# Kernel optimization log

Hardware: AMD Instinct MI355X
Metric: run time of the kernel (lower is better)

## Reference

```python
import jax, jax.numpy as jnp
import numpy as np

BATCH, N, NX, NU, NY = 64, 4096, 128, 32, 32


def setup_inputs() -> dict:
    key = jax.random.key(0)
    k1, k2, k3, k4, k5 = jax.random.split(key, 5)
    # A scaled to spectral radius ~0.9 so the recurrence is stable (module has is_stable()).
    A = jax.random.normal(k1, (NX, NX), jnp.float32) * (0.9 / np.sqrt(NX).astype(np.float32))
    B = jax.random.normal(k2, (NX, NU), jnp.float32) * (1.0 / np.sqrt(NU).astype(np.float32))
    C = jax.random.normal(k3, (NY, NX), jnp.float32) * (1.0 / np.sqrt(NX).astype(np.float32))
    D = jax.random.normal(k4, (NY, NU), jnp.float32) * (1.0 / np.sqrt(NU).astype(np.float32))
    d = jax.random.normal(k5, (BATCH, N, NU, 1), jnp.float32)
    return {"d": d, "A": A, "B": B, "C": C, "D": D}


def reference(d, A, B, C, D):
    # d: [batch, N, nu, 1]. LTI recurrence: x_{k+1} = A x_k + B u_k ; y_k = C x_k + D u_k, x_0 = 0.
    u = jnp.swapaxes(d[..., 0], 0, 1)  # [N, batch, nu] time-major for scan
    x0 = jnp.zeros((d.shape[0], A.shape[0]), d.dtype)  # [batch, nx]

    def step(x, uk):
        y = x @ C.T + uk @ D.T          # [batch, ny] uses pre-update state x_k
        x_next = x @ A.T + uk @ B.T     # [batch, nx]
        return x_next, (y, x)

    xN, (ys, xs) = jax.lax.scan(step, x0, u)
    y = jnp.swapaxes(ys, 0, 1)[..., None]                      # [batch, N, ny, 1]
    x = jnp.swapaxes(xs, 0, 1)                                 # [batch, N, nx] = x_0..x_{N-1}
    x = jnp.concatenate([x, xN[:, None]], axis=1)[..., None]   # [batch, N+1, nx, 1]
    return y, (x,)
```

## Files before the change

### kernel.cpp

```cpp
#include <hip/hip_runtime.h>
#include <stdint.h>
#include <stddef.h>

typedef short s8v   __attribute__((ext_vector_type(8)));
typedef float f32x4 __attribute__((ext_vector_type(4)));

union BF8 { s8v v; unsigned short u[8]; };

__device__ __forceinline__ float bf16_f(unsigned short h) {
  unsigned u = ((unsigned)h) << 16;
  return __builtin_bit_cast(float, u);
}
__device__ __forceinline__ void split_trunc(float x, unsigned short &h, unsigned short &l) {
  unsigned u = __builtin_bit_cast(unsigned, x);
  h = (unsigned short)(u >> 16);
  float hi = __builtin_bit_cast(float, u & 0xFFFF0000u);
  float r = x - hi;
  l = (unsigned short)(__builtin_bit_cast(unsigned, r) >> 16);
}
__device__ __forceinline__ f32x4 mfma16(s8v a, s8v b, f32x4 c) {
  return __builtin_amdgcn_mfma_f32_16x16x32_bf16(a, b, c, 0, 0, 0);
}
__device__ __forceinline__ void split8(f32x4 a, f32x4 b, s8v &h, s8v &l) {
  BF8 hh, ll;
  #pragma unroll
  for (int i = 0; i < 4; ++i) { split_trunc(a[i], hh.u[i], ll.u[i]); split_trunc(b[i], hh.u[4 + i], ll.u[4 + i]); }
  h = hh.v; l = ll.v;
}

#define BATCH 64
#define NN    4096
#define NX    128
#define NU    32
#define NY    32
#define LPAD  132
#define CH    32
#define CPB   128

#define OFF_AH   0
#define OFF_AL   32768
#define OFF_BH   65536
#define OFF_BL   73728
#define OFF_CH   81920
#define OFF_CL   90112
#define OFF_DH   98304
#define OFF_DL   100352
#define OFF_A2H  102400
#define OFF_A2L  135168
#define OFF_ABH  167936
#define OFF_ABL  176128
#define OFF_G1H  184320
#define OFF_G1L  217088
#define OFF_G2H  249856
#define OFF_G2L  282624
#define OFF_G3H  315392
#define OFF_G3L  348160
#define OFF_P0   380928
#define OFF_P1   446464
#define OFF_V    512000
#define OFF_S    4706304

__global__ void k_mm_conv(const float* __restrict__ A, const float* __restrict__ B,
                          const float* __restrict__ C, const float* __restrict__ D,
                          float* __restrict__ P, unsigned short* A2h, unsigned short* A2l,
                          unsigned short* Ah, unsigned short* Al,
                          unsigned short* Bh, unsigned short* Bl,
                          unsigned short* Ch, unsigned short* Cl,
                          unsigned short* Dh, unsigned short* Dl) {
  int gid = blockIdx.x * 256 + threadIdx.x;
  if (blockIdx.x < 64) {
    int row = gid >> 7, col = gid & 127;
    const float* xr = A + row * 128;
    float a0 = 0.f, a1 = 0.f;
    #pragma unroll 8
    for (int k = 0; k < 128; k += 2) {
      a0 = fmaf(xr[k],     A[k * 128 + col],       a0);
      a1 = fmaf(xr[k + 1], A[(k + 1) * 128 + col], a1);
    }
    float acc = a0 + a1;
    P[gid] = acc;
    unsigned short h, l; split_trunc(acc, h, l);
    A2h[gid] = h; A2l[gid] = l;
  } else {
    int idx = gid - 16384;
    unsigned short h, l;
    if (idx < 16384)      { split_trunc(A[idx], h, l); Ah[idx] = h; Al[idx] = l; }
    else if (idx < 20480) { int i = idx - 16384; split_trunc(B[i], h, l); Bh[i] = h; Bl[i] = l; }
    else if (idx < 24576) { int i = idx - 20480; split_trunc(C[i], h, l); Ch[i] = h; Cl[i] = l; }
    else if (idx < 25600) { int i = idx - 24576; split_trunc(D[i], h, l); Dh[i] = h; Dl[i] = l; }
  }
}

__global__ void k_mm128(const float* __restrict__ X, const float* __restrict__ Y,
                        float* __restrict__ Z, unsigned short* Zh, unsigned short* Zl,
                        int writeBF) {
  int gid = blockIdx.x * 256 + threadIdx.x;
  int row = gid >> 7, col = gid & 127;
  const float* xr = X + row * 128;
  float a0 = 0.f, a1 = 0.f;
  #pragma unroll 8
  for (int k = 0; k < 128; k += 2) {
    a0 = fmaf(xr[k],     Y[k * 128 + col],       a0);
    a1 = fmaf(xr[k + 1], Y[(k + 1) * 128 + col], a1);
  }
  float acc = a0 + a1;
  Z[gid] = acc;
  if (writeBF) { unsigned short h, l; split_trunc(acc, h, l); Zh[gid] = h; Zl[gid] = l; }
}

__global__ void k_ab(const float* __restrict__ A, const float* __restrict__ B,
                     unsigned short* ABh, unsigned short* ABl) {
  int gid = blockIdx.x * 256 + threadIdx.x;
  int row = gid >> 5, col = gid & 31;
  float acc = 0.f;
  #pragma unroll 8
  for (int k = 0; k < 128; ++k) acc = fmaf(A[row * 128 + k], B[k * 32 + col], acc);
  unsigned short h, l; split_trunc(acc, h, l);
  ABh[gid] = h; ABl[gid] = l;
}

__global__ __launch_bounds__(256, 2) void k_pass1(
    const float* __restrict__ d,
    const unsigned short* __restrict__ A2h, const unsigned short* __restrict__ A2l,
    const unsigned short* __restrict__ ABh, const unsigned short* __restrict__ ABl,
    const unsigned short* __restrict__ Bh,  const unsigned short* __restrict__ Bl,
    float* __restrict__ vout) {
  __shared__ unsigned short Xh[2][16][LPAD];
  __shared__ unsigned short Xl[2][16][LPAD];
  const int tid = threadIdx.x;
  const int w = tid >> 6, l = tid & 63, q = l >> 4, m = l & 15;
  const int g = blockIdx.x;

  s8v fA2h[2][4], fA2l[2][4], fABh[2], fABl[2], fBh[2], fBl[2];
  #pragma unroll
  for (int t2 = 0; t2 < 2; ++t2) {
    const int n = (2 * w + t2) * 16 + m;
    #pragma unroll
    for (int kt = 0; kt < 4; ++kt) {
      const int k0 = kt * 32 + q * 8;
      fA2h[t2][kt] = *(const s8v*)(A2h + n * 128 + k0);
      fA2l[t2][kt] = *(const s8v*)(A2l + n * 128 + k0);
    }
    fABh[t2] = *(const s8v*)(ABh + n * 32 + q * 8);
    fABl[t2] = *(const s8v*)(ABl + n * 32 + q * 8);
    fBh[t2]  = *(const s8v*)(Bh  + n * 32 + q * 8);
    fBl[t2]  = *(const s8v*)(Bl  + n * 32 + q * 8);
  }
  for (int i = tid; i < 16 * LPAD; i += 256) {
    ((unsigned short*)Xh[0])[i] = 0;
    ((unsigned short*)Xl[0])[i] = 0;
  }
  __syncthreads();

  const int ch = g * 16 + m, b = ch >> 7, chunk = ch & (CPB - 1);
  const float* ubase = d + ((size_t)b * NN + chunk * CH) * NU + q * 8;

  f32x4 cu[4];
  cu[0] = *(const f32x4*)(ubase);      cu[1] = *(const f32x4*)(ubase + 4);
  cu[2] = *(const f32x4*)(ubase + 32); cu[3] = *(const f32x4*)(ubase + 36);

  f32x4 acc[2];
  #pragma unroll 2
  for (int r = 0; r < 16; ++r) {
    const int p = r & 1;
    f32x4 nu0 = cu[0], nu1 = cu[1], nu2 = cu[2], nu3 = cu[3];
    if (r < 15) {
      const float* up = ubase + (size_t)(2 * r + 2) * NU;
      nu0 = *(const f32x4*)up;        nu1 = *(const f32x4*)(up + 4);
      nu2 = *(const f32x4*)(up + 32); nu3 = *(const f32x4*)(up + 36);
    }
    s8v u0h, u0l, u1h, u1l;
    split8(cu[0], cu[1], u0h, u0l);
    split8(cu[2], cu[3], u1h, u1l);
    s8v fXh[4], fXl[4];
    #pragma unroll
    for (int kt = 0; kt < 4; ++kt) {
      fXh[kt] = *(const s8v*)&Xh[p][m][kt * 32 + q * 8];
      fXl[kt] = *(const s8v*)&Xl[p][m][kt * 32 + q * 8];
    }
    #pragma unroll
    for (int t2 = 0; t2 < 2; ++t2) {
      f32x4 a0 = {0.f,0.f,0.f,0.f}, a1 = {0.f,0.f,0.f,0.f}, a2 = {0.f,0.f,0.f,0.f};
      #pragma unroll
      for (int kt = 0; kt < 4; ++kt) a0 = mfma16(fXh[kt], fA2h[t2][kt], a0);
      a0 = mfma16(u0h, fABh[t2], a0);
      a0 = mfma16(u1h, fBh[t2],  a0);
      #pragma unroll
      for (int kt = 0; kt < 4; ++kt) a1 = mfma16(fXl[kt], fA2h[t2][kt], a1);
      a1 = mfma16(u0l, fABh[t2], a1);
      a1 = mfma16(u1l, fBh[t2],  a1);
      #pragma unroll
      for (int kt = 0; kt < 4; ++kt) a2 = mfma16(fXh[kt], fA2l[t2][kt], a2);
      a2 = mfma16(u0h, fABl[t2], a2);
      a2 = mfma16(u1h, fBl[t2],  a2);
      acc[t2] = a0 + a1 + a2;
    }
    if (r < 15) {
      #pragma unroll
      for (int t2 = 0; t2 < 2; ++t2) {
        const int col = (2 * w + t2) * 16 + m;
        #pragma unroll
        for (int rr = 0; rr < 4; ++rr) {
          unsigned short h, lo;
          split_trunc(acc[t2][rr], h, lo);
          Xh[1 - p][q * 4 + rr][col] = h;
          Xl[1 - p][q * 4 + rr][col] = lo;
        }
      }
      __syncthreads();
      cu[0] = nu0; cu[1] = nu1; cu[2] = nu2; cu[3] = nu3;
    }
  }
  #pragma unroll
  for (int t2 = 0; t2 < 2; ++t2) {
    const int col = (2 * w + t2) * 16 + m;
    #pragma unroll
    for (int rr = 0; rr < 4; ++rr) {
      const int row = g * 16 + q * 4 + rr;
      vout[(size_t)row * 128 + col] = acc[t2][rr];
    }
  }
}

__global__ __launch_bounds__(256, 1) void k_carry(
    const unsigned short* __restrict__ G1h, const unsigned short* __restrict__ G1l,
    const unsigned short* __restrict__ G2h, const unsigned short* __restrict__ G2l,
    const unsigned short* __restrict__ G3h, const unsigned short* __restrict__ G3l,
    const float* __restrict__ v, float* __restrict__ sout) {
  const int tid = threadIdx.x;
  const int w = tid >> 6, l = tid & 63, q = l >> 4, m = l & 15;
  const int g = blockIdx.x;
  const int chm = g * 16 + m, cm = chm & (CPB - 1);

  f32x4 a[2];
  a[0] = (f32x4){0.f,0.f,0.f,0.f};
  a[1] = (f32x4){0.f,0.f,0.f,0.f};

#define CARRY_TERM(GH, GL, DELTA)                                              \
  {                                                                            \
    const s8v zero = {0,0,0,0,0,0,0,0};                                        \
    s8v vh[4], vl[4];                                                          \
    _Pragma("unroll")                                                          \
    for (int kt = 0; kt < 4; ++kt) {                                           \
      if (cm >= DELTA) {                                                       \
        const float* vp = v + (size_t)(chm - DELTA) * NX + kt * 32 + q * 8;    \
        split8(*(const f32x4*)vp, *(const f32x4*)(vp + 4), vh[kt], vl[kt]);    \
      } else { vh[kt] = zero; vl[kt] = zero; }                                 \
    }                                                                          \
    _Pragma("unroll")                                                          \
    for (int t2 = 0; t2 < 2; ++t2) {                                           \
      const int n = (2 * w + t2) * 16 + m;                                     \
      _Pragma("unroll")                                                        \
      for (int kt = 0; kt < 4; ++kt) {                                         \
        const int k0 = kt * 32 + q * 8;                                        \
        s8v gh = *(const s8v*)(GH + n * NX + k0);                              \
        s8v gl = *(const s8v*)(GL + n * NX + k0);                              \
        a[t2] = mfma16(vh[kt], gh, a[t2]);                                     \
        a[t2] = mfma16(vl[kt], gh, a[t2]);                                     \
        a[t2] = mfma16(vh[kt], gl, a[t2]);                                     \
      }                                                                        \
    }                                                                          \
  }

  CARRY_TERM(G1h, G1l, 2)
  CARRY_TERM(G2h, G2l, 3)
  CARRY_TERM(G3h, G3l, 4)
#undef CARRY_TERM

  #pragma unroll
  for (int t2 = 0; t2 < 2; ++t2) {
    const int col = (2 * w + t2) * 16 + m;
    #pragma unroll
    for (int rr = 0; rr < 4; ++rr) {
      const int chr = g * 16 + q * 4 + rr, cr = chr & (CPB - 1);
      float sv = 0.f;
      if (cr >= 1) sv = a[t2][rr] + v[(size_t)(chr - 1) * NX + col];
      sout[(size_t)chr * NX + col] = sv;
    }
  }
}

__global__ __launch_bounds__(256, 2) void k_scan2(
    const float* __restrict__ d, const float* __restrict__ s,
    const unsigned short* __restrict__ Ah, const unsigned short* __restrict__ Al,
    const unsigned short* __restrict__ Bh, const unsigned short* __restrict__ Bl,
    const unsigned short* __restrict__ Ch, const unsigned short* __restrict__ Cl,
    const unsigned short* __restrict__ Dh, const unsigned short* __restrict__ Dl,
    float* __restrict__ yout, float* __restrict__ xout) {
  __shared__ unsigned short Eh[16][LPAD];
  __shared__ unsigned short El[16][LPAD];
  __shared__ unsigned short Oh[16][LPAD];
  __shared__ unsigned short Ol[16][LPAD];
  const int tid = threadIdx.x;
  const int w = tid >> 6, l = tid & 63, q = l >> 4, m = l & 15;
  const int g = blockIdx.x;

  s8v fAh[2][4], fAl[2][4], fBh[2], fBl[2];
  #pragma unroll
  for (int t2 = 0; t2 < 2; ++t2) {
    const int n = (2 * w + t2) * 16 + m;
    #pragma unroll
    for (int kt = 0; kt < 4; ++kt) {
      const int k0 = kt * 32 + q * 8;
      fAh[t2][kt] = *(const s8v*)(Ah + n * 128 + k0);
      fAl[t2][kt] = *(const s8v*)(Al + n * 128 + k0);
    }
    fBh[t2] = *(const s8v*)(Bh + n * 32 + q * 8);
    fBl[t2] = *(const s8v*)(Bl + n * 32 + q * 8);
  }
  s8v fCh[4], fCl[4], fDh, fDl;
  {
    const int o = (w & 1) * 16 + m;
    #pragma unroll
    for (int kt = 0; kt < 4; ++kt) {
      const int k0 = kt * 32 + q * 8;
      fCh[kt] = *(const s8v*)(Ch + o * 128 + k0);
      fCl[kt] = *(const s8v*)(Cl + o * 128 + k0);
    }
    fDh = *(const s8v*)(Dh + o * 32 + q * 8);
    fDl = *(const s8v*)(Dl + o * 32 + q * 8);
  }

  {
    const int lb = tid >> 4, i0 = (tid & 15) * 8;
    const int chS = g * 16 + lb, bS = chS >> 7, cS = chS & (CPB - 1);
    const float* sp = s + (size_t)chS * 128 + i0;
    f32x4 s0 = *(const f32x4*)sp, s1 = *(const f32x4*)(sp + 4);
    s8v hh, ll;
    split8(s0, s1, hh, ll);
    *(s8v*)&Eh[lb][i0] = hh;
    *(s8v*)&El[lb][i0] = ll;
    float* xp = xout + ((size_t)bS * (NN + 1) + (size_t)cS * CH) * NX + i0;
    *(f32x4*)xp = s0;
    *(f32x4*)(xp + 4) = s1;
  }
  __syncthreads();

  const int ch = g * 16 + m, b = ch >> 7, chunk = ch & (CPB - 1);
  const float* ubase = d + ((size_t)b * NN + chunk * CH) * NU + q * 8;

  float* xptr[2][4];
  bool xlast[2][4];
  float* yptr[4];
  #pragma unroll
  for (int t2 = 0; t2 < 2; ++t2) {
    const int col = (2 * w + t2) * 16 + m;
    #pragma unroll
    for (int rr = 0; rr < 4; ++rr) {
      const int chX = g * 16 + q * 4 + rr, bX = chX >> 7, cX = chX & (CPB - 1);
      xptr[t2][rr] = xout + ((size_t)bX * (NN + 1) + (size_t)cX * CH + 1) * NX + col;
      xlast[t2][rr] = (cX == CPB - 1);
    }
  }
  #pragma unroll
  for (int rr = 0; rr < 4; ++rr) {
    const int chY = g * 16 + q * 4 + rr, bY = chY >> 7, cY = chY & (CPB - 1);
    yptr[rr] = yout + ((size_t)bY * NN + (size_t)cY * CH) * NY + (w & 1) * 16 + m;
  }

  f32x4 cu[4];
  cu[0] = *(const f32x4*)(ubase);      cu[1] = *(const f32x4*)(ubase + 4);
  cu[2] = *(const f32x4*)(ubase + 32); cu[3] = *(const f32x4*)(ubase + 36);

  #pragma unroll 1
  for (int r = 0; r < 16; ++r) {
    f32x4 nu0 = cu[0], nu1 = cu[1], nu2 = cu[2], nu3 = cu[3];
    if (r < 15) {
      const float* up = ubase + (size_t)(2 * r + 2) * NU;
      nu0 = *(const f32x4*)up;        nu1 = *(const f32x4*)(up + 4);
      nu2 = *(const f32x4*)(up + 32); nu3 = *(const f32x4*)(up + 36);
    }
    s8v u0h, u0l;
    split8(cu[0], cu[1], u0h, u0l);
    s8v fXh[4], fXl[4];
    #pragma unroll
    for (int kt = 0; kt < 4; ++kt) {
      fXh[kt] = *(const s8v*)&Eh[m][kt * 32 + q * 8];
      fXl[kt] = *(const s8v*)&El[m][kt * 32 + q * 8];
    }
    f32x4 xo[2];
    #pragma unroll
    for (int t2 = 0; t2 < 2; ++t2) {
      f32x4 a0 = {0.f,0.f,0.f,0.f}, a1 = {0.f,0.f,0.f,0.f}, a2 = {0.f,0.f,0.f,0.f};
      #pragma unroll
      for (int kt = 0; kt < 4; ++kt) a0 = mfma16(fXh[kt], fAh[t2][kt], a0);
      a0 = mfma16(u0h, fBh[t2], a0);
      #pragma unroll
      for (int kt = 0; kt < 4; ++kt) a1 = mfma16(fXl[kt], fAh[t2][kt], a1);
      a1 = mfma16(u0l, fBh[t2], a1);
      #pragma unroll
      for (int kt = 0; kt < 4; ++kt) a2 = mfma16(fXh[kt], fAl[t2][kt], a2);
      a2 = mfma16(u0h, fBl[t2], a2);
      xo[t2] = a0 + a1 + a2;
    }
    if (w < 2) {
      f32x4 b0 = {0.f,0.f,0.f,0.f}, b1 = {0.f,0.f,0.f,0.f}, b2 = {0.f,0.f,0.f,0.f};
      #pragma unroll
      for (int kt = 0; kt < 4; ++kt) b0 = mfma16(fXh[kt], fCh[kt], b0);
      b0 = mfma16(u0h, fDh, b0);
      #pragma unroll
      for (int kt = 0; kt < 4; ++kt) b1 = mfma16(fXl[kt], fCh[kt], b1);
      b1 = mfma16(u0l, fDh, b1);
      #pragma unroll
      for (int kt = 0; kt < 4; ++kt) b2 = mfma16(fXh[kt], fCl[kt], b2);
      b2 = mfma16(u0h, fDl, b2);
      f32x4 yv = b0 + b1 + b2;
      #pragma unroll
      for (int rr = 0; rr < 4; ++rr) *(yptr[rr]) = yv[rr];
    }
    #pragma unroll
    for (int t2 = 0; t2 < 2; ++t2) {
      const int col = (2 * w + t2) * 16 + m;
      #pragma unroll
      for (int rr = 0; rr < 4; ++rr) {
        *(xptr[t2][rr]) = xo[t2][rr];
        unsigned short h, lo;
        split_trunc(xo[t2][rr], h, lo);
        Oh[q * 4 + rr][col] = h;
        Ol[q * 4 + rr][col] = lo;
      }
    }
    __syncthreads();

    s8v u1h, u1l;
    split8(cu[2], cu[3], u1h, u1l);
    s8v fOh[4], fOl[4];
    #pragma unroll
    for (int kt = 0; kt < 4; ++kt) {
      fOh[kt] = *(const s8v*)&Oh[m][kt * 32 + q * 8];
      fOl[kt] = *(const s8v*)&Ol[m][kt * 32 + q * 8];
    }
    f32x4 xe[2];
    #pragma unroll
    for (int t2 = 0; t2 < 2; ++t2) {
      f32x4 a0 = {0.f,0.f,0.f,0.f}, a1 = {0.f,0.f,0.f,0.f}, a2 = {0.f,0.f,0.f,0.f};
      #pragma unroll
      for (int kt = 0; kt < 4; ++kt) a0 = mfma16(fOh[kt], fAh[t2][kt], a0);
      a0 = mfma16(u1h, fBh[t2], a0);
      #pragma unroll
      for (int kt = 0; kt < 4; ++kt) a1 = mfma16(fOl[kt], fAh[t2][kt], a1);
      a1 = mfma16(u1l, fBh[t2], a1);
      #pragma unroll
      for (int kt = 0; kt < 4; ++kt) a2 = mfma16(fOh[kt], fAl[t2][kt], a2);
      a2 = mfma16(u1h, fBl[t2], a2);
      xe[t2] = a0 + a1 + a2;
    }
    if (w >= 2) {
      f32x4 c0 = {0.f,0.f,0.f,0.f}, c1 = {0.f,0.f,0.f,0.f}, c2 = {0.f,0.f,0.f,0.f};
      #pragma unroll
      for (int kt = 0; kt < 4; ++kt) c0 = mfma16(fOh[kt], fCh[kt], c0);
      c0 = mfma16(u1h, fDh, c0);
      #pragma unroll
      for (int kt = 0; kt < 4; ++kt) c1 = mfma16(fOl[kt], fCh[kt], c1);
      c1 = mfma16(u1l, fDh, c1);
      #pragma unroll
      for (int kt = 0; kt < 4; ++kt) c2 = mfma16(fOh[kt], fCl[kt], c2);
      c2 = mfma16(u1h, fDl, c2);
      f32x4 yv = c0 + c1 + c2;
      #pragma unroll
      for (int rr = 0; rr < 4; ++rr) *(yptr[rr] + NY) = yv[rr];
    }
    #pragma unroll
    for (int t2 = 0; t2 < 2; ++t2) {
      const int col = (2 * w + t2) * 16 + m;
      #pragma unroll
      for (int rr = 0; rr < 4; ++rr) {
        if (r < 15 || xlast[t2][rr]) *(xptr[t2][rr] + NX) = xe[t2][rr];
        unsigned short h, lo;
        split_trunc(xe[t2][rr], h, lo);
        Eh[q * 4 + rr][col] = h;
        El[q * 4 + rr][col] = lo;
      }
    }
    __syncthreads();

    if (r < 15) {
      cu[0] = nu0; cu[1] = nu1; cu[2] = nu2; cu[3] = nu3;
      #pragma unroll
      for (int t2 = 0; t2 < 2; ++t2)
        #pragma unroll
        for (int rr = 0; rr < 4; ++rr) xptr[t2][rr] += 2 * NX;
      #pragma unroll
      for (int rr = 0; rr < 4; ++rr) yptr[rr] += 2 * NY;
    }
  }
}

extern "C" void kernel_launch(void* const* d_in, const int* in_sizes, int n_in,
                              void* d_out, int out_size, void* d_ws, size_t ws_size,
                              hipStream_t stream) {
  (void)in_sizes; (void)n_in; (void)out_size; (void)ws_size;
  const float* d = (const float*)d_in[0];
  const float* A = (const float*)d_in[1];
  const float* B = (const float*)d_in[2];
  const float* C = (const float*)d_in[3];
  const float* D = (const float*)d_in[4];

  char* ws = (char*)d_ws;
  unsigned short* Ah  = (unsigned short*)(ws + OFF_AH);
  unsigned short* Al  = (unsigned short*)(ws + OFF_AL);
  unsigned short* Bh  = (unsigned short*)(ws + OFF_BH);
  unsigned short* Bl  = (unsigned short*)(ws + OFF_BL);
  unsigned short* Chp = (unsigned short*)(ws + OFF_CH);
  unsigned short* Clp = (unsigned short*)(ws + OFF_CL);
  unsigned short* Dhp = (unsigned short*)(ws + OFF_DH);
  unsigned short* Dlp = (unsigned short*)(ws + OFF_DL);
  unsigned short* A2h = (unsigned short*)(ws + OFF_A2H);
  unsigned short* A2l = (unsigned short*)(ws + OFF_A2L);
  unsigned short* ABh = (unsigned short*)(ws + OFF_ABH);
  unsigned short* ABl = (unsigned short*)(ws + OFF_ABL);
  unsigned short* G1h = (unsigned short*)(ws + OFF_G1H);
  unsigned short* G1l = (unsigned short*)(ws + OFF_G1L);
  unsigned short* G2h = (unsigned short*)(ws + OFF_G2H);
  unsigned short* G2l = (unsigned short*)(ws + OFF_G2L);
  unsigned short* G3h = (unsigned short*)(ws + OFF_G3H);
  unsigned short* G3l = (unsigned short*)(ws + OFF_G3L);
  float* P0 = (float*)(ws + OFF_P0);
  float* P1 = (float*)(ws + OFF_P1);
  float* V  = (float*)(ws + OFF_V);
  float* S  = (float*)(ws + OFF_S);

  float* yout = (float*)d_out;
  float* xout = yout + (size_t)BATCH * NN * NY;

  k_mm_conv<<<164, 256, 0, stream>>>(A, B, C, D, P0, A2h, A2l,
                                     Ah, Al, Bh, Bl, Chp, Clp, Dhp, Dlp);
  k_ab<<<16, 256, 0, stream>>>(A, B, ABh, ABl);
  k_mm128<<<64, 256, 0, stream>>>(P0, P0, P1, nullptr, nullptr, 0);
  k_mm128<<<64, 256, 0, stream>>>(P1, P1, P0, nullptr, nullptr, 0);
  k_mm128<<<64, 256, 0, stream>>>(P0, P0, P1, nullptr, nullptr, 0);
  k_mm128<<<64, 256, 0, stream>>>(P1, P1, P0, G1h, G1l, 1);
  k_mm128<<<64, 256, 0, stream>>>(P0, P0, P1, G2h, G2l, 1);
  k_mm128<<<64, 256, 0, stream>>>(P0, P1, V,  G3h, G3l, 1);

  k_pass1<<<512, 256, 0, stream>>>(d, A2h, A2l, ABh, ABl, Bh, Bl, V);
  k_carry<<<512, 256, 0, stream>>>(G1h, G1l, G2h, G2l, G3h, G3l, V, S);
  k_scan2<<<512, 256, 0, stream>>>(d, S, Ah, Al, Bh, Bl, Chp, Clp, Dhp, Dlp,
                                   yout, xout);
}
```

Before: 290.3 us.

## Pre-split input into bf16 hi/lo buffers in a merged prep kernel

Adds a prep stage that converts the whole input d into bf16 hi/lo arrays once, and merges the old conversion and A*B kernels into that single launch. Both scan kernels now load pre-split u fragments, so the per-step split arithmetic inside the serial recurrence loops goes away. The cost is an extra full pass over d plus writing two bf16 copies, which keeps total traffic about the same but moves work off the latency-bound loops. k_carry's launch bounds are also raised to allow two blocks per CU.

```diff
diff --git a/kernel.cpp b/kernel.cpp
--- a/kernel.cpp
+++ b/kernel.cpp
@@ -59,16 +59,31 @@
 #define OFF_P1   446464
 #define OFF_V    512000
 #define OFF_S    4706304
-
-__global__ void k_mm_conv(const float* __restrict__ A, const float* __restrict__ B,
-                          const float* __restrict__ C, const float* __restrict__ D,
-                          float* __restrict__ P, unsigned short* A2h, unsigned short* A2l,
-                          unsigned short* Ah, unsigned short* Al,
-                          unsigned short* Bh, unsigned short* Bl,
-                          unsigned short* Ch, unsigned short* Cl,
-                          unsigned short* Dh, unsigned short* Dl) {
-  int gid = blockIdx.x * 256 + threadIdx.x;
-  if (blockIdx.x < 64) {
+#define OFF_UH   8900608
+#define OFF_UL   25677824
+
+__global__ void k_prep(const float* __restrict__ A, const float* __restrict__ B,
+                       const float* __restrict__ C, const float* __restrict__ D,
+                       const float* __restrict__ d,
+                       float* __restrict__ P, unsigned short* A2h, unsigned short* A2l,
+                       unsigned short* Ah, unsigned short* Al,
+                       unsigned short* Bh, unsigned short* Bl,
+                       unsigned short* Ch, unsigned short* Cl,
+                       unsigned short* Dh, unsigned short* Dl,
+                       unsigned short* ABh, unsigned short* ABl,
+                       unsigned short* Uh, unsigned short* Ul) {
+  const int blk = blockIdx.x;
+  if (blk >= 180) {
+    const size_t i0 = ((size_t)(blk - 180) * 256 + threadIdx.x) * 8;
+    f32x4 a = *(const f32x4*)(d + i0);
+    f32x4 b = *(const f32x4*)(d + i0 + 4);
+    s8v h, l; split8(a, b, h, l);
+    *(s8v*)(Uh + i0) = h;
+    *(s8v*)(Ul + i0) = l;
+    return;
+  }
+  int gid = blk * 256 + threadIdx.x;
+  if (blk < 64) {
     int row = gid >> 7, col = gid & 127;
     const float* xr = A + row * 128;
     float a0 = 0.f, a1 = 0.f;
@@ -81,13 +96,21 @@
     P[gid] = acc;
     unsigned short h, l; split_trunc(acc, h, l);
     A2h[gid] = h; A2l[gid] = l;
-  } else {
+  } else if (blk < 164) {
     int idx = gid - 16384;
     unsigned short h, l;
     if (idx < 16384)      { split_trunc(A[idx], h, l); Ah[idx] = h; Al[idx] = l; }
     else if (idx < 20480) { int i = idx - 16384; split_trunc(B[i], h, l); Bh[i] = h; Bl[i] = l; }
     else if (idx < 24576) { int i = idx - 20480; split_trunc(C[i], h, l); Ch[i] = h; Cl[i] = l; }
     else if (idx < 25600) { int i = idx - 24576; split_trunc(D[i], h, l); Dh[i] = h; Dl[i] = l; }
+  } else {
+    int i = gid - 41984;
+    int row = i >> 5, col = i & 31;
+    float acc = 0.f;
+    #pragma unroll 8
+    for (int k = 0; k < 128; ++k) acc = fmaf(A[row * 128 + k], B[k * 32 + col], acc);
+    unsigned short h, l; split_trunc(acc, h, l);
+    ABh[i] = h; ABl[i] = l;
   }
 }
 
@@ -108,19 +131,8 @@
   if (writeBF) { unsigned short h, l; split_trunc(acc, h, l); Zh[gid] = h; Zl[gid] = l; }
 }
 
-__global__ void k_ab(const float* __restrict__ A, const float* __restrict__ B,
-                     unsigned short* ABh, unsigned short* ABl) {
-  int gid = blockIdx.x * 256 + threadIdx.x;
-  int row = gid >> 5, col = gid & 31;
-  float acc = 0.f;
-  #pragma unroll 8
-  for (int k = 0; k < 128; ++k) acc = fmaf(A[row * 128 + k], B[k * 32 + col], acc);
-  unsigned short h, l; split_trunc(acc, h, l);
-  ABh[gid] = h; ABl[gid] = l;
-}
-
 __global__ __launch_bounds__(256, 2) void k_pass1(
-    const float* __restrict__ d,
+    const unsigned short* __restrict__ Uh, const unsigned short* __restrict__ Ul,
     const unsigned short* __restrict__ A2h, const unsigned short* __restrict__ A2l,
     const unsigned short* __restrict__ ABh, const unsigned short* __restrict__ ABl,
     const unsigned short* __restrict__ Bh,  const unsigned short* __restrict__ Bl,
@@ -153,25 +165,23 @@
   __syncthreads();
 
   const int ch = g * 16 + m, b = ch >> 7, chunk = ch & (CPB - 1);
-  const float* ubase = d + ((size_t)b * NN + chunk * CH) * NU + q * 8;
-
-  f32x4 cu[4];
-  cu[0] = *(const f32x4*)(ubase);      cu[1] = *(const f32x4*)(ubase + 4);
-  cu[2] = *(const f32x4*)(ubase + 32); cu[3] = *(const f32x4*)(ubase + 36);
+  const size_t ubase = ((size_t)b * NN + chunk * CH) * NU + q * 8;
+  const unsigned short* uhb = Uh + ubase;
+  const unsigned short* ulb = Ul + ubase;
+
+  s8v u0h = *(const s8v*)(uhb),      u0l = *(const s8v*)(ulb);
+  s8v u1h = *(const s8v*)(uhb + NU), u1l = *(const s8v*)(ulb + NU);
 
   f32x4 acc[2];
   #pragma unroll 2
   for (int r = 0; r < 16; ++r) {
     const int p = r & 1;
-    f32x4 nu0 = cu[0], nu1 = cu[1], nu2 = cu[2], nu3 = cu[3];
+    s8v n0h = u0h, n0l = u0l, n1h = u1h, n1l = u1l;
     if (r < 15) {
-      const float* up = ubase + (size_t)(2 * r + 2) * NU;
-      nu0 = *(const f32x4*)up;        nu1 = *(const f32x4*)(up + 4);
-      nu2 = *(const f32x4*)(up + 32); nu3 = *(const f32x4*)(up + 36);
-    }
-    s8v u0h, u0l, u1h, u1l;
-    split8(cu[0], cu[1], u0h, u0l);
-    split8(cu[2], cu[3], u1h, u1l);
+      const size_t off = (size_t)(2 * r + 2) * NU;
+      n0h = *(const s8v*)(uhb + off);      n0l = *(const s8v*)(ulb + off);
+      n1h = *(const s8v*)(uhb + off + NU); n1l = *(const s8v*)(ulb + off + NU);
+    }
     s8v fXh[4], fXl[4];
     #pragma unroll
     for (int kt = 0; kt < 4; ++kt) {
@@ -208,7 +218,7 @@
         }
       }
       __syncthreads();
-      cu[0] = nu0; cu[1] = nu1; cu[2] = nu2; cu[3] = nu3;
+      u0h = n0h; u0l = n0l; u1h = n1h; u1l = n1l;
     }
   }
   #pragma unroll
@@ -222,7 +232,7 @@
   }
 }
 
-__global__ __launch_bounds__(256, 1) void k_carry(
+__global__ __launch_bounds__(256, 2) void k_carry(
     const unsigned short* __restrict__ G1h, const unsigned short* __restrict__ G1l,
     const unsigned short* __restrict__ G2h, const unsigned short* __restrict__ G2l,
     const unsigned short* __restrict__ G3h, const unsigned short* __restrict__ G3l,
@@ -281,7 +291,8 @@
 }
 
 __global__ __launch_bounds__(256, 2) void k_scan2(
-    const float* __restrict__ d, const float* __restrict__ s,
+    const unsigned short* __restrict__ Uh, const unsigned short* __restrict__ Ul,
+    const float* __restrict__ s,
     const unsigned short* __restrict__ Ah, const unsigned short* __restrict__ Al,
     const unsigned short* __restrict__ Bh, const unsigned short* __restrict__ Bl,
     const unsigned short* __restrict__ Ch, const unsigned short* __restrict__ Cl,
@@ -337,7 +348,9 @@
   __syncthreads();
 
   const int ch = g * 16 + m, b = ch >> 7, chunk = ch & (CPB - 1);
-  const float* ubase = d + ((size_t)b * NN + chunk * CH) * NU + q * 8;
+  const size_t ubase = ((size_t)b * NN + chunk * CH) * NU + q * 8;
+  const unsigned short* uhb = Uh + ubase;
+  const unsigned short* ulb = Ul + ubase;
 
   float* xptr[2][4];
   bool xlast[2][4];
@@ -358,20 +371,17 @@
     yptr[rr] = yout + ((size_t)bY * NN + (size_t)cY * CH) * NY + (w & 1) * 16 + m;
   }
 
-  f32x4 cu[4];
-  cu[0] = *(const f32x4*)(ubase);      cu[1] = *(const f32x4*)(ubase + 4);
-  cu[2] = *(const f32x4*)(ubase + 32); cu[3] = *(const f32x4*)(ubase + 36);
+  s8v u0h = *(const s8v*)(uhb),      u0l = *(const s8v*)(ulb);
+  s8v u1h = *(const s8v*)(uhb + NU), u1l = *(const s8v*)(ulb + NU);
 
   #pragma unroll 1
   for (int r = 0; r < 16; ++r) {
-    f32x4 nu0 = cu[0], nu1 = cu[1], nu2 = cu[2], nu3 = cu[3];
+    s8v n0h = u0h, n0l = u0l, n1h = u1h, n1l = u1l;
     if (r < 15) {
-      const float* up = ubase + (size_t)(2 * r + 2) * NU;
-      nu0 = *(const f32x4*)up;        nu1 = *(const f32x4*)(up + 4);
-      nu2 = *(const f32x4*)(up + 32); nu3 = *(const f32x4*)(up + 36);
-    }
-    s8v u0h, u0l;
-    split8(cu[0], cu[1], u0h, u0l);
+      const size_t off = (size_t)(2 * r + 2) * NU;
+      n0h = *(const s8v*)(uhb + off);      n0l = *(const s8v*)(ulb + off);
+      n1h = *(const s8v*)(uhb + off + NU); n1l = *(const s8v*)(ulb + off + NU);
+    }
     s8v fXh[4], fXl[4];
     #pragma unroll
     for (int kt = 0; kt < 4; ++kt) {
@@ -422,8 +432,6 @@
     }
     __syncthreads();
 
-    s8v u1h, u1l;
-    split8(cu[2], cu[3], u1h, u1l);
     s8v fOh[4], fOl[4];
     #pragma unroll
     for (int kt = 0; kt < 4; ++kt) {
@@ -475,7 +483,7 @@
     __syncthreads();
 
     if (r < 15) {
-      cu[0] = nu0; cu[1] = nu1; cu[2] = nu2; cu[3] = nu3;
+      u0h = n0h; u0l = n0l; u1h = n1h; u1l = n1l;
       #pragma unroll
       for (int t2 = 0; t2 < 2; ++t2)
         #pragma unroll
@@ -515,6 +523,8 @@
   unsigned short* G2l = (unsigned short*)(ws + OFF_G2L);
   unsigned short* G3h = (unsigned short*)(ws + OFF_G3H);
   unsigned short* G3l = (unsigned short*)(ws + OFF_G3L);
+  unsigned short* Uh  = (unsigned short*)(ws + OFF_UH);
+  unsigned short* Ul  = (unsigned short*)(ws + OFF_UL);
   float* P0 = (float*)(ws + OFF_P0);
   float* P1 = (float*)(ws + OFF_P1);
   float* V  = (float*)(ws + OFF_V);
@@ -523,9 +533,9 @@
   float* yout = (float*)d_out;
   float* xout = yout + (size_t)BATCH * NN * NY;
 
-  k_mm_conv<<<164, 256, 0, stream>>>(A, B, C, D, P0, A2h, A2l,
-                                     Ah, Al, Bh, Bl, Chp, Clp, Dhp, Dlp);
-  k_ab<<<16, 256, 0, stream>>>(A, B, ABh, ABl);
+  k_prep<<<4276, 256, 0, stream>>>(A, B, C, D, d, P0, A2h, A2l,
+                                   Ah, Al, Bh, Bl, Chp, Clp, Dhp, Dlp,
+                                   ABh, ABl, Uh, Ul);
   k_mm128<<<64, 256, 0, stream>>>(P0, P0, P1, nullptr, nullptr, 0);
   k_mm128<<<64, 256, 0, stream>>>(P1, P1, P0, nullptr, nullptr, 0);
   k_mm128<<<64, 256, 0, stream>>>(P0, P0, P1, nullptr, nullptr, 0);
@@ -533,8 +543,8 @@
   k_mm128<<<64, 256, 0, stream>>>(P0, P0, P1, G2h, G2l, 1);
   k_mm128<<<64, 256, 0, stream>>>(P0, P1, V,  G3h, G3l, 1);
 
-  k_pass1<<<512, 256, 0, stream>>>(d, A2h, A2l, ABh, ABl, Bh, Bl, V);
+  k_pass1<<<512, 256, 0, stream>>>(Uh, Ul, A2h, A2l, ABh, ABl, Bh, Bl, V);
   k_carry<<<512, 256, 0, stream>>>(G1h, G1l, G2h, G2l, G3h, G3l, V, S);
-  k_scan2<<<512, 256, 0, stream>>>(d, S, Ah, Al, Bh, Bl, Chp, Clp, Dhp, Dlp,
+  k_scan2<<<512, 256, 0, stream>>>(Uh, Ul, S, Ah, Al, Bh, Bl, Chp, Clp, Dhp, Dlp,
                                    yout, xout);
 }
```

Result: no change. 295.0 us (+1.6%).
